# Kernel tuning notes

Measured on AMD Instinct MI355X. Metric: run time of the kernel, lower is better.

The kernel has to match this reference:

```python
import jax, jax.numpy as jnp
import numpy as np

GROUP_SIZES = [16, 16, 16, 16]
K = 2
TEMPERATURE = 1.0
NEG = float(np.finfo(np.float32).min)  # torch.finfo(dtype).min


def setup_inputs() -> dict:
    key = jax.random.key(0)
    k1, k2, k3 = jax.random.split(key, 3)
    B, S, D, E, G = 8, 4096, 1024, 64, len(GROUP_SIZES)
    x = jax.random.normal(k1, (B, S, D), dtype=jnp.float32)
    W_group = jax.random.normal(k2, (G, D), dtype=jnp.float32) * 0.02
    W_expert = jax.random.normal(k3, (E, D), dtype=jnp.float32) * 0.02
    return {"x": x, "W_group": W_group, "W_expert": W_expert}


def reference(x, W_group, W_expert):
    E = W_expert.shape[0]
    # group id of each expert (contiguous ranges) -- static
    expert_group = jnp.asarray(np.repeat(np.arange(len(GROUP_SIZES)), GROUP_SIZES))  # [E]

    # gate logits (no bias), temperature scaling
    expert_logits = jnp.einsum('bsd,ed->bse', x, W_expert) * (1.0 / TEMPERATURE)  # [B,S,E]
    group_logits = jnp.einsum('bsd,gd->bsg', x, W_group)                          # [B,S,G]
    group_probs = jax.nn.softmax(group_logits, axis=-1)
    g_idx = jnp.argmax(group_probs, axis=-1)                                      # [B,S]

    # mask experts outside the selected group's contiguous range
    mask = expert_group[None, None, :] != g_idx[..., None]                        # [B,S,E] bool
    mdt = mask.astype(expert_logits.dtype)
    masked_logits = mdt * NEG + (1.0 - mdt) * expert_logits

    probs_full = jax.nn.softmax(masked_logits, axis=-1)                           # [B,S,E]
    topk_vals, idx = jax.lax.top_k(masked_logits, K)                              # [B,S,K]
    scores = jax.nn.softmax(topk_vals, axis=-1)

    # aux stats (no_grad in original)
    importance = jax.lax.stop_gradient(jnp.mean(probs_full, axis=(0, 1)))         # [E]
    counts = jnp.zeros((E,), probs_full.dtype).at[idx.reshape(-1)].add(1.0)       # [E]
    load = counts / jnp.maximum(jnp.sum(counts), 1.0)
    return (idx, scores, probs_full, importance, load)
```

## Files before the change

### kernel.cpp

```cpp
#include <hip/hip_runtime.h>
#include <math.h>

#define TOKENS   32768
#define DDIM     1024
#define TPB      16
#define NBLOCKS  (TOKENS / TPB)

#define OFF_SCORES 65536
#define OFF_PROBS  131072
#define OFF_IMP    2228224
#define OFF_LOAD   2228288

#define NSLOT 16

typedef __attribute__((ext_vector_type(8))) short  short8;
typedef __attribute__((ext_vector_type(4))) float  f32x4;
typedef __attribute__((ext_vector_type(4))) int    intx4;

__device__ __attribute__((aligned(16))) short wfrag[32 * 5 * 3 * 64 * 8];

__device__ inline unsigned rne_hi(float x) {
  unsigned u = __float_as_uint(x);
  unsigned r = u + 0x7fffu + ((u >> 16) & 1u);
  return r & 0xffff0000u;
}

__device__ inline void split3(const float* xv, short8& f1, short8& f2, short8& f3) {
  int o1[4], o2[4], o3[4];
  #pragma unroll
  for (int p = 0; p < 4; ++p) {
    float x0 = xv[2*p], x1 = xv[2*p+1];
    unsigned h0 = rne_hi(x0), h1 = rne_hi(x1);
    o1[p] = (int)((h0 >> 16) | (h1 & 0xffff0000u));
    float r0 = x0 - __uint_as_float(h0);
    float r1 = x1 - __uint_as_float(h1);
    unsigned g0 = rne_hi(r0), g1 = rne_hi(r1);
    o2[p] = (int)((g0 >> 16) | (g1 & 0xffff0000u));
    float s0 = r0 - __uint_as_float(g0);
    float s1 = r1 - __uint_as_float(g1);
    unsigned w0 = rne_hi(s0), w1 = rne_hi(s1);
    o3[p] = (int)((w0 >> 16) | (w1 & 0xffff0000u));
  }
  intx4 t1 = {o1[0], o1[1], o1[2], o1[3]};
  intx4 t2 = {o2[0], o2[1], o2[2], o2[3]};
  intx4 t3 = {o3[0], o3[1], o3[2], o3[3]};
  f1 = __builtin_bit_cast(short8, t1);
  f2 = __builtin_bit_cast(short8, t2);
  f3 = __builtin_bit_cast(short8, t3);
}

__global__ void prep_kernel(const float* __restrict__ Wg, const float* __restrict__ We) {
  const int nt   = blockIdx.x >> 5;
  const int ks   = blockIdx.x & 31;
  const int lane = threadIdx.x & 63;
  const int row  = nt * 16 + (lane & 15);
  const int k0   = ks * 32 + (lane >> 4) * 8;
  float xv[8];
  #pragma unroll
  for (int j = 0; j < 8; ++j) {
    float v = 0.f;
    if (row < 64)      v = We[(size_t)row * DDIM + k0 + j];
    else if (row < 68) v = Wg[(size_t)(row - 64) * DDIM + k0 + j];
    xv[j] = v;
  }
  short8 f1, f2, f3;
  split3(xv, f1, f2, f3);
  short8* dst = (short8*)wfrag + (((size_t)ks * 5 + nt) * 3) * 64 + lane;
  dst[0]   = f1;
  dst[64]  = f2;
  dst[128] = f3;
}

__global__ __launch_bounds__(128, 4)
void router_kernel(const float* __restrict__ x,
                   float* __restrict__ out,
                   float* __restrict__ ws) {
  __shared__ __attribute__((aligned(16))) float el[TPB * 88];
  __shared__ int cnt[64];
  const int tid    = threadIdx.x;
  const int lane   = tid & 63;
  const int khalf  = tid >> 6;
  const int quad   = lane >> 4;
  const int m      = lane & 15;
  const int tokblk = blockIdx.x * TPB;

  if (tid < 64) cnt[tid] = 0;

  const float* ap0 = x + (size_t)(tokblk + m) * DDIM + khalf * 512 + quad * 8;

  f32x4 ahi[5], alo[5];
  #pragma unroll
  for (int nt = 0; nt < 5; ++nt) { ahi[nt] = 0.f; alo[nt] = 0.f; }

  for (int ks = 0; ks < 16; ++ks) {
    const float* p0 = ap0 + ks * 32;
    float4 a0 = *(const float4*)(p0), a1 = *(const float4*)(p0 + 4);

    const short8* bp = (const short8*)wfrag + ((size_t)(khalf * 16 + ks) * 15) * 64 + lane;
    short8 fb[5][3];
    #pragma unroll
    for (int nt = 0; nt < 5; ++nt) {
      fb[nt][0] = bp[nt * 192];
      fb[nt][1] = bp[nt * 192 + 64];
      fb[nt][2] = bp[nt * 192 + 128];
    }
    short8 fa[3];
    {
      float av[8] = {a0.x, a0.y, a0.z, a0.w, a1.x, a1.y, a1.z, a1.w};
      split3(av, fa[0], fa[1], fa[2]);
    }
    #pragma unroll
    for (int nt = 0; nt < 5; ++nt) {
      ahi[nt] = __builtin_amdgcn_mfma_f32_16x16x32_bf16(fa[0], fb[nt][0], ahi[nt], 0, 0, 0);
      f32x4 c = alo[nt];
      c = __builtin_amdgcn_mfma_f32_16x16x32_bf16(fa[0], fb[nt][1], c, 0, 0, 0);
      c = __builtin_amdgcn_mfma_f32_16x16x32_bf16(fa[1], fb[nt][0], c, 0, 0, 0);
      c = __builtin_amdgcn_mfma_f32_16x16x32_bf16(fa[1], fb[nt][1], c, 0, 0, 0);
      c = __builtin_amdgcn_mfma_f32_16x16x32_bf16(fa[0], fb[nt][2], c, 0, 0, 0);
      c = __builtin_amdgcn_mfma_f32_16x16x32_bf16(fa[2], fb[nt][0], c, 0, 0, 0);
      c = __builtin_amdgcn_mfma_f32_16x16x32_bf16(fa[1], fb[nt][2], c, 0, 0, 0);
      c = __builtin_amdgcn_mfma_f32_16x16x32_bf16(fa[2], fb[nt][1], c, 0, 0, 0);
      alo[nt] = c;
    }
  }

  if (khalf == 1) {
    #pragma unroll
    for (int nt = 0; nt < 5; ++nt)
      #pragma unroll
      for (int r = 0; r < 4; ++r)
        el[(quad * 4 + r) * 88 + nt * 16 + m] = ahi[nt][r] + alo[nt][r];
  }
  __syncthreads();
  if (khalf == 0) {
    #pragma unroll
    for (int nt = 0; nt < 5; ++nt)
      #pragma unroll
      for (int r = 0; r < 4; ++r) {
        const int idx = (quad * 4 + r) * 88 + nt * 16 + m;
        el[idx] += ahi[nt][r] + alo[nt][r];
      }
  }
  __syncthreads();

  if (tid < TPB) {
    const int t = tid;
    float* row = el + t * 88;
    const float g0 = row[64], g1 = row[65], g2 = row[66], g3 = row[67];
    int g = 0; float gb = g0;
    if (g1 > gb) { g = 1; gb = g1; }
    if (g2 > gb) { g = 2; gb = g2; }
    if (g3 > gb) { g = 3; gb = g3; }
    const int base = g << 4;
    float l[16];
    #pragma unroll
    for (int e = 0; e < 16; ++e) l[e] = row[base + e];
    int i1 = 0; float v1 = l[0];
    #pragma unroll
    for (int e = 1; e < 16; ++e) if (l[e] > v1) { i1 = e; v1 = l[e]; }
    int i2 = -1; float v2 = 0.f;
    #pragma unroll
    for (int e = 0; e < 16; ++e) {
      if (e == i1) continue;
      if (i2 < 0 || l[e] > v2) { i2 = e; v2 = l[e]; }
    }
    float pr[16]; float s = 0.f;
    #pragma unroll
    for (int e = 0; e < 16; ++e) { pr[e] = expf(l[e] - v1); s += pr[e]; }
    const float inv = 1.f / s;
    #pragma unroll
    for (int c = 0; c < 64; ++c) row[c] = 0.f;
    #pragma unroll
    for (int e = 0; e < 16; ++e) row[base + e] = pr[e] * inv;
    const size_t T = (size_t)tokblk + t;
    out[2*T]     = (float)(base + i1);
    out[2*T + 1] = (float)(base + i2);
    const float e2 = expf(v2 - v1);
    const float si = 1.f / (1.f + e2);
    out[OFF_SCORES + 2*T]     = si;
    out[OFF_SCORES + 2*T + 1] = e2 * si;
    atomicAdd(&cnt[base + i1], 1);
    atomicAdd(&cnt[base + i2], 1);
  }
  __syncthreads();

  for (int i = tid; i < TPB * 64; i += 128) {
    const int t = i >> 6, c = i & 63;
    out[OFF_PROBS + (((size_t)(tokblk + t)) << 6) + c] = el[t * 88 + c];
  }
  if (tid < 64) {
    const int e = tid;
    float s = 0.f;
    #pragma unroll 4
    for (int t = 0; t < TPB; ++t) s += el[t * 88 + e];
    const int slot = (blockIdx.x & (NSLOT - 1)) * 128;
    atomicAdd(&ws[slot + e], s);
    atomicAdd(&ws[slot + 64 + e], (float)cnt[e]);
  }
}

__global__ void finalize_kernel(const float* __restrict__ ws, float* __restrict__ out) {
  const int e = threadIdx.x;
  if (e < 64) {
    float imp = 0.f, cf = 0.f;
    #pragma unroll
    for (int s = 0; s < NSLOT; ++s) {
      imp += ws[s * 128 + e];
      cf  += ws[s * 128 + 64 + e];
    }
    out[OFF_IMP  + e] = imp * (1.0f / 32768.0f);
    out[OFF_LOAD + e] = cf  * (1.0f / 65536.0f);
  }
}

extern "C" void kernel_launch(void* const* d_in, const int* in_sizes, int n_in,
                              void* d_out, int out_size, void* d_ws, size_t ws_size,
                              hipStream_t stream) {
  (void)in_sizes; (void)n_in; (void)out_size; (void)ws_size;
  const float* x  = (const float*)d_in[0];
  const float* Wg = (const float*)d_in[1];
  const float* We = (const float*)d_in[2];
  float* out = (float*)d_out;
  float* ws  = (float*)d_ws;
  hipMemsetAsync(d_ws, 0, NSLOT * 128 * sizeof(float), stream);
  hipLaunchKernelGGL(prep_kernel, dim3(160), dim3(64), 0, stream, Wg, We);
  hipLaunchKernelGGL(router_kernel, dim3(NBLOCKS), dim3(128), 0, stream, x, out, ws);
  hipLaunchKernelGGL(finalize_kernel, dim3(1), dim3(64), 0, stream, ws, out);
}
```

Measured before the change: 243.4 us.

## Process two 16-token M tiles per block and prefetch next x slice

Doubles tokens per block so each loaded weight fragment feeds MFMAs for two token tiles, halving weight-fragment loads per token. It also software-prefetches the next k-step's x values into registers while the current step computes. Register pressure roughly doubles for the accumulators, so launch bounds drop to 2 blocks per CU, which lowers occupancy. The epilogue indexing is extended to 32 rows, and the shared el buffer grows with TPB.

```diff
diff --git a/kernel.cpp b/kernel.cpp
--- a/kernel.cpp
+++ b/kernel.cpp
@@ -3,7 +3,7 @@
 
 #define TOKENS   32768
 #define DDIM     1024
-#define TPB      16
+#define TPB      32
 #define NBLOCKS  (TOKENS / TPB)
 
 #define OFF_SCORES 65536
@@ -71,7 +71,7 @@
   dst[128] = f3;
 }
 
-__global__ __launch_bounds__(128, 4)
+__global__ __launch_bounds__(128, 2)
 void router_kernel(const float* __restrict__ x,
                    float* __restrict__ out,
                    float* __restrict__ ws) {
@@ -87,15 +87,18 @@
   if (tid < 64) cnt[tid] = 0;
 
   const float* ap0 = x + (size_t)(tokblk + m) * DDIM + khalf * 512 + quad * 8;
-
-  f32x4 ahi[5], alo[5];
+  const float* ap1 = ap0 + (size_t)16 * DDIM;
+
+  f32x4 ahi[2][5], alo[2][5];
   #pragma unroll
-  for (int nt = 0; nt < 5; ++nt) { ahi[nt] = 0.f; alo[nt] = 0.f; }
+  for (int mt = 0; mt < 2; ++mt)
+    #pragma unroll
+    for (int nt = 0; nt < 5; ++nt) { ahi[mt][nt] = 0.f; alo[mt][nt] = 0.f; }
+
+  float4 a0 = *(const float4*)(ap0), a1 = *(const float4*)(ap0 + 4);
+  float4 a2 = *(const float4*)(ap1), a3 = *(const float4*)(ap1 + 4);
 
   for (int ks = 0; ks < 16; ++ks) {
-    const float* p0 = ap0 + ks * 32;
-    float4 a0 = *(const float4*)(p0), a1 = *(const float4*)(p0 + 4);
-
     const short8* bp = (const short8*)wfrag + ((size_t)(khalf * 16 + ks) * 15) * 64 + lane;
     short8 fb[5][3];
     #pragma unroll
@@ -104,42 +107,58 @@
       fb[nt][1] = bp[nt * 192 + 64];
       fb[nt][2] = bp[nt * 192 + 128];
     }
-    short8 fa[3];
+    float4 n0, n1, n2, n3;
+    if (ks < 15) {
+      const float* p0 = ap0 + (ks + 1) * 32;
+      const float* p1 = ap1 + (ks + 1) * 32;
+      n0 = *(const float4*)(p0);  n1 = *(const float4*)(p0 + 4);
+      n2 = *(const float4*)(p1);  n3 = *(const float4*)(p1 + 4);
+    }
+    short8 fa[2][3];
     {
       float av[8] = {a0.x, a0.y, a0.z, a0.w, a1.x, a1.y, a1.z, a1.w};
-      split3(av, fa[0], fa[1], fa[2]);
-    }
-    #pragma unroll
-    for (int nt = 0; nt < 5; ++nt) {
-      ahi[nt] = __builtin_amdgcn_mfma_f32_16x16x32_bf16(fa[0], fb[nt][0], ahi[nt], 0, 0, 0);
-      f32x4 c = alo[nt];
-      c = __builtin_amdgcn_mfma_f32_16x16x32_bf16(fa[0], fb[nt][1], c, 0, 0, 0);
-      c = __builtin_amdgcn_mfma_f32_16x16x32_bf16(fa[1], fb[nt][0], c, 0, 0, 0);
-      c = __builtin_amdgcn_mfma_f32_16x16x32_bf16(fa[1], fb[nt][1], c, 0, 0, 0);
-      c = __builtin_amdgcn_mfma_f32_16x16x32_bf16(fa[0], fb[nt][2], c, 0, 0, 0);
-      c = __builtin_amdgcn_mfma_f32_16x16x32_bf16(fa[2], fb[nt][0], c, 0, 0, 0);
-      c = __builtin_amdgcn_mfma_f32_16x16x32_bf16(fa[1], fb[nt][2], c, 0, 0, 0);
-      c = __builtin_amdgcn_mfma_f32_16x16x32_bf16(fa[2], fb[nt][1], c, 0, 0, 0);
-      alo[nt] = c;
-    }
-  }
-
-  if (khalf == 1) {
+      split3(av, fa[0][0], fa[0][1], fa[0][2]);
+      float bv[8] = {a2.x, a2.y, a2.z, a2.w, a3.x, a3.y, a3.z, a3.w};
+      split3(bv, fa[1][0], fa[1][1], fa[1][2]);
+    }
     #pragma unroll
     for (int nt = 0; nt < 5; ++nt)
       #pragma unroll
-      for (int r = 0; r < 4; ++r)
-        el[(quad * 4 + r) * 88 + nt * 16 + m] = ahi[nt][r] + alo[nt][r];
+      for (int mt = 0; mt < 2; ++mt) {
+        ahi[mt][nt] = __builtin_amdgcn_mfma_f32_16x16x32_bf16(fa[mt][0], fb[nt][0], ahi[mt][nt], 0, 0, 0);
+        f32x4 c = alo[mt][nt];
+        c = __builtin_amdgcn_mfma_f32_16x16x32_bf16(fa[mt][0], fb[nt][1], c, 0, 0, 0);
+        c = __builtin_amdgcn_mfma_f32_16x16x32_bf16(fa[mt][1], fb[nt][0], c, 0, 0, 0);
+        c = __builtin_amdgcn_mfma_f32_16x16x32_bf16(fa[mt][1], fb[nt][1], c, 0, 0, 0);
+        c = __builtin_amdgcn_mfma_f32_16x16x32_bf16(fa[mt][0], fb[nt][2], c, 0, 0, 0);
+        c = __builtin_amdgcn_mfma_f32_16x16x32_bf16(fa[mt][2], fb[nt][0], c, 0, 0, 0);
+        c = __builtin_amdgcn_mfma_f32_16x16x32_bf16(fa[mt][1], fb[nt][2], c, 0, 0, 0);
+        c = __builtin_amdgcn_mfma_f32_16x16x32_bf16(fa[mt][2], fb[nt][1], c, 0, 0, 0);
+        alo[mt][nt] = c;
+      }
+    a0 = n0; a1 = n1; a2 = n2; a3 = n3;
+  }
+
+  if (khalf == 1) {
+    #pragma unroll
+    for (int mt = 0; mt < 2; ++mt)
+      #pragma unroll
+      for (int nt = 0; nt < 5; ++nt)
+        #pragma unroll
+        for (int r = 0; r < 4; ++r)
+          el[(mt * 16 + quad * 4 + r) * 88 + nt * 16 + m] = ahi[mt][nt][r] + alo[mt][nt][r];
   }
   __syncthreads();
   if (khalf == 0) {
     #pragma unroll
-    for (int nt = 0; nt < 5; ++nt)
+    for (int mt = 0; mt < 2; ++mt)
       #pragma unroll
-      for (int r = 0; r < 4; ++r) {
-        const int idx = (quad * 4 + r) * 88 + nt * 16 + m;
-        el[idx] += ahi[nt][r] + alo[nt][r];
-      }
+      for (int nt = 0; nt < 5; ++nt)
+        #pragma unroll
+        for (int r = 0; r < 4; ++r) {
+          const int idx = (mt * 16 + quad * 4 + r) * 88 + nt * 16 + m;
+          el[idx] += ahi[mt][nt][r] + alo[mt][nt][r];
+        }
   }
   __syncthreads();
 
```

Result: faster. 217.4 us (-10.7%).

## Double 32-token blocks across four waves and prefetch x and weight fragments

Applied to the files above, without the earlier changes.

Each block now handles 32 tokens with four waves: two token tiles times two K halves. Block count halves and each block reuses the weight fragments across more tokens. The K loop is software-pipelined: the next x chunk and the next weight-fragment triplet are loaded while the current MFMAs run, replacing the bulk load of all fragments. This raises register pressure and occupancy changes under the new launch bounds of 256 threads with 3 blocks.

```diff
diff --git a/kernel.cpp b/kernel.cpp
--- a/kernel.cpp
+++ b/kernel.cpp
@@ -3,7 +3,7 @@
 
 #define TOKENS   32768
 #define DDIM     1024
-#define TPB      16
+#define TPB      32
 #define NBLOCKS  (TOKENS / TPB)
 
 #define OFF_SCORES 65536
@@ -71,7 +71,7 @@
   dst[128] = f3;
 }
 
-__global__ __launch_bounds__(128, 4)
+__global__ __launch_bounds__(256, 3)
 void router_kernel(const float* __restrict__ x,
                    float* __restrict__ out,
                    float* __restrict__ ws) {
@@ -79,30 +79,31 @@
   __shared__ int cnt[64];
   const int tid    = threadIdx.x;
   const int lane   = tid & 63;
-  const int khalf  = tid >> 6;
+  const int wv     = tid >> 6;
+  const int mt     = wv & 1;
+  const int khalf  = wv >> 1;
   const int quad   = lane >> 4;
   const int m      = lane & 15;
   const int tokblk = blockIdx.x * TPB;
 
   if (tid < 64) cnt[tid] = 0;
 
-  const float* ap0 = x + (size_t)(tokblk + m) * DDIM + khalf * 512 + quad * 8;
+  const float* ap = x + (size_t)(tokblk + mt * 16 + m) * DDIM + khalf * 512 + quad * 8;
 
   f32x4 ahi[5], alo[5];
   #pragma unroll
   for (int nt = 0; nt < 5; ++nt) { ahi[nt] = 0.f; alo[nt] = 0.f; }
 
+  const short8* bbase = (const short8*)wfrag + ((size_t)(khalf * 16) * 15) * 64 + lane;
+  float4 a0 = *(const float4*)(ap), a1 = *(const float4*)(ap + 4);
+  short8 b0 = bbase[0], b1 = bbase[64], b2 = bbase[128];
+
   for (int ks = 0; ks < 16; ++ks) {
-    const float* p0 = ap0 + ks * 32;
-    float4 a0 = *(const float4*)(p0), a1 = *(const float4*)(p0 + 4);
-
-    const short8* bp = (const short8*)wfrag + ((size_t)(khalf * 16 + ks) * 15) * 64 + lane;
-    short8 fb[5][3];
-    #pragma unroll
-    for (int nt = 0; nt < 5; ++nt) {
-      fb[nt][0] = bp[nt * 192];
-      fb[nt][1] = bp[nt * 192 + 64];
-      fb[nt][2] = bp[nt * 192 + 128];
+    const short8* bp = bbase + (size_t)ks * 15 * 64;
+    float4 n0, n1;
+    if (ks < 15) {
+      const float* p = ap + (ks + 1) * 32;
+      n0 = *(const float4*)(p);  n1 = *(const float4*)(p + 4);
     }
     short8 fa[3];
     {
@@ -111,17 +112,27 @@
     }
     #pragma unroll
     for (int nt = 0; nt < 5; ++nt) {
-      ahi[nt] = __builtin_amdgcn_mfma_f32_16x16x32_bf16(fa[0], fb[nt][0], ahi[nt], 0, 0, 0);
+      short8 c0, c1, c2;
+      if (nt < 4) {
+        c0 = bp[(nt + 1) * 192];
+        c1 = bp[(nt + 1) * 192 + 64];
+        c2 = bp[(nt + 1) * 192 + 128];
+      } else if (ks < 15) {
+        c0 = bp[15 * 64];  c1 = bp[15 * 64 + 64];  c2 = bp[15 * 64 + 128];
+      }
+      ahi[nt] = __builtin_amdgcn_mfma_f32_16x16x32_bf16(fa[0], b0, ahi[nt], 0, 0, 0);
       f32x4 c = alo[nt];
-      c = __builtin_amdgcn_mfma_f32_16x16x32_bf16(fa[0], fb[nt][1], c, 0, 0, 0);
-      c = __builtin_amdgcn_mfma_f32_16x16x32_bf16(fa[1], fb[nt][0], c, 0, 0, 0);
-      c = __builtin_amdgcn_mfma_f32_16x16x32_bf16(fa[1], fb[nt][1], c, 0, 0, 0);
-      c = __builtin_amdgcn_mfma_f32_16x16x32_bf16(fa[0], fb[nt][2], c, 0, 0, 0);
-      c = __builtin_amdgcn_mfma_f32_16x16x32_bf16(fa[2], fb[nt][0], c, 0, 0, 0);
-      c = __builtin_amdgcn_mfma_f32_16x16x32_bf16(fa[1], fb[nt][2], c, 0, 0, 0);
-      c = __builtin_amdgcn_mfma_f32_16x16x32_bf16(fa[2], fb[nt][1], c, 0, 0, 0);
+      c = __builtin_amdgcn_mfma_f32_16x16x32_bf16(fa[0], b1, c, 0, 0, 0);
+      c = __builtin_amdgcn_mfma_f32_16x16x32_bf16(fa[1], b0, c, 0, 0, 0);
+      c = __builtin_amdgcn_mfma_f32_16x16x32_bf16(fa[1], b1, c, 0, 0, 0);
+      c = __builtin_amdgcn_mfma_f32_16x16x32_bf16(fa[0], b2, c, 0, 0, 0);
+      c = __builtin_amdgcn_mfma_f32_16x16x32_bf16(fa[2], b0, c, 0, 0, 0);
+      c = __builtin_amdgcn_mfma_f32_16x16x32_bf16(fa[1], b2, c, 0, 0, 0);
+      c = __builtin_amdgcn_mfma_f32_16x16x32_bf16(fa[2], b1, c, 0, 0, 0);
       alo[nt] = c;
-    }
+      b0 = c0; b1 = c1; b2 = c2;
+    }
+    a0 = n0; a1 = n1;
   }
 
   if (khalf == 1) {
@@ -129,7 +140,7 @@
     for (int nt = 0; nt < 5; ++nt)
       #pragma unroll
       for (int r = 0; r < 4; ++r)
-        el[(quad * 4 + r) * 88 + nt * 16 + m] = ahi[nt][r] + alo[nt][r];
+        el[(mt * 16 + quad * 4 + r) * 88 + nt * 16 + m] = ahi[nt][r] + alo[nt][r];
   }
   __syncthreads();
   if (khalf == 0) {
@@ -137,7 +148,7 @@
     for (int nt = 0; nt < 5; ++nt)
       #pragma unroll
       for (int r = 0; r < 4; ++r) {
-        const int idx = (quad * 4 + r) * 88 + nt * 16 + m;
+        const int idx = (mt * 16 + quad * 4 + r) * 88 + nt * 16 + m;
         el[idx] += ahi[nt][r] + alo[nt][r];
       }
   }
@@ -184,7 +195,7 @@
   }
   __syncthreads();
 
-  for (int i = tid; i < TPB * 64; i += 128) {
+  for (int i = tid; i < TPB * 64; i += 256) {
     const int t = i >> 6, c = i & 63;
     out[OFF_PROBS + (((size_t)(tokblk + t)) << 6) + c] = el[t * 88 + c];
   }
@@ -224,6 +235,6 @@
   float* ws  = (float*)d_ws;
   hipMemsetAsync(d_ws, 0, NSLOT * 128 * sizeof(float), stream);
   hipLaunchKernelGGL(prep_kernel, dim3(160), dim3(64), 0, stream, Wg, We);
-  hipLaunchKernelGGL(router_kernel, dim3(NBLOCKS), dim3(128), 0, stream, x, out, ws);
+  hipLaunchKernelGGL(router_kernel, dim3(NBLOCKS), dim3(256), 0, stream, x, out, ws);
   hipLaunchKernelGGL(finalize_kernel, dim3(1), dim3(64), 0, stream, ws, out);
 }
```

Result: no change. 244.6 us (+0.5%).
